# Optimization experiments

Measured on AMD Instinct MI355X. Metric: run time of the kernel, lower is better.

## Reference

```python
import jax, jax.numpy as jnp
import numpy as np
from jax import lax

B_COEF = np.array([0.0048243445989025905, 0.019297378395610362, 0.028946067593415543,
                   0.019297378395610362, 0.0048243445989025905], dtype=np.float32)
A_COEF = np.array([1.0, -2.369513007182038, 2.3139884144002064,
                   -1.0546654058785661, 0.18737949236818502], dtype=np.float32)


def setup_inputs() -> dict:
    key = jax.random.key(0)
    x = jax.random.normal(key, (32, 16, 32768), dtype=jnp.float32)
    return {"x": x, "b": jnp.asarray(B_COEF), "a": jnp.asarray(A_COEF)}


def _odd_ext(x, n):
    left = 2.0 * x[..., :1] - x[..., 1:n + 1][..., ::-1]
    right = 2.0 * x[..., -1:] - x[..., -(n + 1):-1][..., ::-1]
    return jnp.concatenate([left, x, right], axis=-1)


def _lfilter(x, b, a):
    # Direct form II transposed IIR, zero initial conditions.
    # x: [N, T]; b, a: [K]
    b = b / a[0]
    a = a / a[0]
    K = b.shape[0]

    def step(z, xt):  # z: [N, K-1], xt: [N]
        y = b[0] * xt + z[:, 0]
        z_shift = jnp.pad(z[:, 1:], ((0, 0), (0, 1)))
        z_new = b[1:] * xt[:, None] - a[1:] * y[:, None] + z_shift
        return z_new, y

    z0 = jnp.zeros((x.shape[0], K - 1), dtype=x.dtype)
    _, y = lax.scan(step, z0, x.T)  # y: [T, N]
    return y.T


def _filtfilt(x, b, a):
    # torchaudio-style filtfilt: forward lfilter, then backward lfilter (zero ICs).
    y = _lfilter(x, b, a)
    y = _lfilter(y[:, ::-1], b, a)[:, ::-1]
    return y


def reference(x, b, a):
    scale = jnp.max(jnp.abs(x), axis=-1, keepdims=True)
    xn = x / scale
    padlen = 3 * max(a.shape[0], b.shape[0])  # static: 15
    xe = _odd_ext(xn, padlen)                 # [B, C, T + 2*padlen]
    shp = xe.shape
    y = _filtfilt(xe.reshape(-1, shp[-1]), b, a)
    y = y.reshape(shp)[..., padlen:-padlen]
    return y * scale
```

## Files before the change

### kernel.cpp

```cpp
#include <hip/hip_runtime.h>


typedef __fp16 h2 __attribute__((ext_vector_type(2)));
typedef __fp16 h4 __attribute__((ext_vector_type(4)));
typedef __fp16 h8 __attribute__((ext_vector_type(8)));

constexpr int kT      = 32768;
constexpr int kSeg    = 2048;
constexpr int kNSeg   = kT / kSeg;
constexpr int kTPB    = 256;
constexpr int kSliceB = 4224;

#define B0 0.0048243445989025905f
#define B1 0.019297378395610362f
#define B2 0.028946067593415543f
#define B3 0.019297378395610362f
#define B4 0.0048243445989025905f
#define NA1 2.369513007182038f
#define NA2 (-2.3139884144002064f)
#define NA3 1.0546654058785661f
#define NA4 (-0.18737949236818502f)

#define STEPF(xv) do { \
    y  = fmaf(B0, (xv), z1); \
    z1 = fmaf(NA1, y, fmaf(B1, (xv), z2)); \
    z2 = fmaf(NA2, y, fmaf(B2, (xv), z3)); \
    z3 = fmaf(NA3, y, fmaf(B3, (xv), z4)); \
    z4 = fmaf(NA4, y, B4 * (xv)); \
} while (0)

#define PK(a, b) __builtin_bit_cast(int, __builtin_amdgcn_cvt_pkrtz((a), (b)))

__device__ __forceinline__ int swz(int lo) { return lo ^ (((lo >> 7) & 7) << 4); }

__global__ __launch_bounds__(kTPB, 4)
void filtfilt_kernel(const float* __restrict__ x, float* __restrict__ out) {
    __shared__ __align__(16) char lds[4 * kSliceB];
    const int t  = threadIdx.x;
    const int l  = t & 63;
    const int wv = t >> 6;
    const int W  = blockIdx.x * 4 + wv;
    const int row = W >> 4;
    const int seg = W & (kNSeg - 1);
    const float* __restrict__ xr   = x   + (size_t)row * kT + seg * kSeg;
    float* __restrict__ outr       = out + (size_t)row * kT + seg * kSeg;
    char* Lb = lds + wv * kSliceB;
    const bool haspre  = (seg > 0);
    const bool haspost = (seg < kNSeg - 1);

    const float4* xp = (const float4*)xr;
    float4 mv[8];
    #pragma unroll
    for (int i = 0; i < 8; ++i) mv[i] = xp[i * 64 + l];
    float4 pre4 = {0.f, 0.f, 0.f, 0.f}, post4 = {0.f, 0.f, 0.f, 0.f};
    if (l < 8) {
        if (haspre)  pre4  = *(const float4*)(xr - 32 + l * 4);
        if (haspost) post4 = *(const float4*)(xr + kSeg + l * 4);
    }
    #pragma unroll
    for (int i = 0; i < 8; ++i) {
        int lo = swz(64 + i * 512 + 8 * l);
        int2 wi = { PK(mv[i].x, mv[i].y), PK(mv[i].z, mv[i].w) };
        *(int2*)(Lb + lo) = wi;
    }
    if (l < 8) {
        if (haspre) {
            int2 wi = { PK(pre4.x, pre4.y), PK(pre4.z, pre4.w) };
            *(int2*)(Lb + 8 * l) = wi;
        }
        if (haspost) {
            int2 wi = { PK(post4.x, post4.y), PK(post4.z, post4.w) };
            *(int2*)(Lb + 4160 + 8 * l) = wi;
        }
    }
    asm volatile("s_waitcnt lgkmcnt(0)" ::: "memory");
    if (!haspre && l < 8) {
        const __fp16* xs = (const __fp16*)(Lb + 64);
        float x0 = (float)xs[0];
        float v[4];
        #pragma unroll
        for (int r = 0; r < 4; ++r) {
            int k = 4 * l + r;
            v[r] = (k < 17) ? 0.f : fmaf(2.f, x0, -(float)xs[32 - k]);
        }
        int2 wi = { PK(v[0], v[1]), PK(v[2], v[3]) };
        *(int2*)(Lb + 8 * l) = wi;
    }
    asm volatile("" ::: "memory");

    float z1 = 0.f, z2 = 0.f, z3 = 0.f, z4 = 0.f, y;
    {
        const int wb = l * 64;
        const int xv = ((wb >> 7) & 7) << 4;
        #pragma unroll
        for (int j = 0; j < 4; ++j) {
            h8 v = *(const h8*)(Lb + ((wb + 16 * j) ^ xv));
            #pragma unroll
            for (int e = 0; e < 8; ++e) STEPF((float)v[e]);
        }
    }

    h8 tailA, tailB;
    {
        const int mb = (l + 1) * 64;
        const int xm = ((mb >> 7) & 7) << 4;
        #pragma unroll
        for (int j = 0; j < 4; ++j) {
            char* p = Lb + ((mb + 16 * j) ^ xm);
            h8 v = *(const h8*)p;
            if (j == 2) tailA = v;
            if (j == 3) tailB = v;
            float q[8];
            #pragma unroll
            for (int e = 0; e < 8; ++e) { STEPF((float)v[e]); q[e] = y; }
            int4 wi = { PK(q[0], q[1]), PK(q[2], q[3]), PK(q[4], q[5]), PK(q[6], q[7]) };
            *(int4*)p = wi;
        }
    }

    if (l == 63) {
        if (haspost) {
            #pragma unroll
            for (int g = 0; g < 4; ++g) {
                h8 v = *(const h8*)(Lb + 4160 + 16 * g);
                if (g < 3) {
                    float q[8];
                    #pragma unroll
                    for (int e = 0; e < 8; ++e) { STEPF((float)v[e]); q[e] = y; }
                    int4 wi = { PK(q[0], q[1]), PK(q[2], q[3]), PK(q[4], q[5]), PK(q[6], q[7]) };
                    *(int4*)(Lb + 4160 + 16 * g) = wi;
                } else {
                    float q[4];
                    #pragma unroll
                    for (int e = 0; e < 4; ++e) { STEPF((float)v[e]); q[e] = y; }
                    int4 wi = { PK(q[0], q[1]), PK(q[2], q[3]), 0, 0 };
                    *(int4*)(Lb + 4160 + 16 * g) = wi;
                }
            }
        } else {
            float xl = (float)tailB[7];
            float q[8];
            #pragma unroll
            for (int j = 0; j < 8; ++j) {
                float xe = fmaf(2.f, xl, -(float)(j < 7 ? tailB[6 - j] : tailA[14 - j]));
                STEPF(xe); q[j] = y;
            }
            int4 w0 = { PK(q[0], q[1]), PK(q[2], q[3]), PK(q[4], q[5]), PK(q[6], q[7]) };
            *(int4*)(Lb + 4160) = w0;
            float r[7];
            #pragma unroll
            for (int j = 8; j < 15; ++j) {
                float xe = fmaf(2.f, xl, -(float)tailA[14 - j]);
                STEPF(xe); r[j - 8] = y;
            }
            int4 w1 = { PK(r[0], r[1]), PK(r[2], r[3]), PK(r[4], r[5]), PK(r[6], 0.f) };
            *(int4*)(Lb + 4176) = w1;
            int4 zz = {0, 0, 0, 0};
            *(int4*)(Lb + 4192) = zz;
            *(int4*)(Lb + 4208) = zz;
        }
    }
    asm volatile("" ::: "memory");

    z1 = z2 = z3 = z4 = 0.f;
    {
        const int bb = (l + 2) * 64;
        const int xb = ((bb >> 7) & 7) << 4;
        h8 w3v = *(const h8*)(Lb + ((bb + 48) ^ xb));
        h8 w2v = *(const h8*)(Lb + ((bb + 32) ^ xb));
        h8 w1v = *(const h8*)(Lb + ((bb + 16) ^ xb));
        h8 w0v = *(const h8*)(Lb + ((bb +  0) ^ xb));
        STEPF((float)w3v[3]); STEPF((float)w3v[2]);
        STEPF((float)w3v[1]); STEPF((float)w3v[0]);
        #pragma unroll
        for (int e = 7; e >= 0; --e) STEPF((float)w2v[e]);
        #pragma unroll
        for (int e = 7; e >= 0; --e) STEPF((float)w1v[e]);
        #pragma unroll
        for (int e = 7; e >= 0; --e) STEPF((float)w0v[e]);
    }

    {
        const int mb = (l + 1) * 64;
        const int xm = ((mb >> 7) & 7) << 4;
        #pragma unroll
        for (int j = 3; j >= 0; --j) {
            char* p = Lb + ((mb + 16 * j) ^ xm);
            h8 v = *(const h8*)p;
            float q[8];
            #pragma unroll
            for (int e = 7; e >= 0; --e) { STEPF((float)v[e]); q[e] = y; }
            int4 wi = { PK(q[0], q[1]), PK(q[2], q[3]), PK(q[4], q[5]), PK(q[6], q[7]) };
            *(int4*)p = wi;
        }
    }
    asm volatile("" ::: "memory");

    float4* op = (float4*)outr;
    #pragma unroll
    for (int i = 0; i < 8; ++i) {
        int lo = swz(64 + i * 512 + 8 * l);
        h4 hv = *(const h4*)(Lb + lo);
        float4 o = { (float)hv[0], (float)hv[1], (float)hv[2], (float)hv[3] };
        op[i * 64 + l] = o;
    }
}

extern "C" void kernel_launch(void* const* d_in, const int* in_sizes, int n_in,
                              void* d_out, int out_size, void* d_ws, size_t ws_size,
                              hipStream_t stream) {
    const float* x = (const float*)d_in[0];
    float* outp    = (float*)d_out;
    const int rows   = in_sizes[0] / kT;
    const int blocks = rows * kNSeg * 64 / kTPB;
    filtfilt_kernel<<<blocks, kTPB, 0, stream>>>(x, outp);
}
```

Measured before the change: 119.6 us.

## Process two segments per wave with second segment's loads issued upfront

Each wavefront now handles two adjacent 2048-sample segments instead of one, halving the grid size. Global loads for both segments are issued before the first segment's filtering so the second segment's memory latency hides behind the first's serial IIR compute. The cost is more live registers (a second set of eight float4 values) and fewer waves in flight, which may reduce occupancy-based latency hiding.

```diff
diff --git a/kernel.cpp b/kernel.cpp
--- a/kernel.cpp
+++ b/kernel.cpp
@@ -1,7 +1,6 @@
 #include <hip/hip_runtime.h>
 
 
-typedef __fp16 h2 __attribute__((ext_vector_type(2)));
 typedef __fp16 h4 __attribute__((ext_vector_type(4)));
 typedef __fp16 h8 __attribute__((ext_vector_type(8)));
 
@@ -33,30 +32,11 @@
 
 __device__ __forceinline__ int swz(int lo) { return lo ^ (((lo >> 7) & 7) << 4); }
 
-__global__ __launch_bounds__(kTPB, 4)
-void filtfilt_kernel(const float* __restrict__ x, float* __restrict__ out) {
-    __shared__ __align__(16) char lds[4 * kSliceB];
-    const int t  = threadIdx.x;
-    const int l  = t & 63;
-    const int wv = t >> 6;
-    const int W  = blockIdx.x * 4 + wv;
-    const int row = W >> 4;
-    const int seg = W & (kNSeg - 1);
-    const float* __restrict__ xr   = x   + (size_t)row * kT + seg * kSeg;
-    float* __restrict__ outr       = out + (size_t)row * kT + seg * kSeg;
-    char* Lb = lds + wv * kSliceB;
-    const bool haspre  = (seg > 0);
-    const bool haspost = (seg < kNSeg - 1);
-
-    const float4* xp = (const float4*)xr;
-    float4 mv[8];
-    #pragma unroll
-    for (int i = 0; i < 8; ++i) mv[i] = xp[i * 64 + l];
-    float4 pre4 = {0.f, 0.f, 0.f, 0.f}, post4 = {0.f, 0.f, 0.f, 0.f};
-    if (l < 8) {
-        if (haspre)  pre4  = *(const float4*)(xr - 32 + l * 4);
-        if (haspost) post4 = *(const float4*)(xr + kSeg + l * 4);
-    }
+__device__ __forceinline__ void process_seg(
+    char* __restrict__ Lb, const int l,
+    const float4 (&mv)[8], const float4 pre4, const float4 post4,
+    const bool haspre, const bool haspost, float* __restrict__ outr)
+{
     #pragma unroll
     for (int i = 0; i < 8; ++i) {
         int lo = swz(64 + i * 512 + 8 * l);
@@ -206,12 +186,53 @@
     }
 }
 
+__global__ __launch_bounds__(kTPB, 4)
+void filtfilt_kernel(const float* __restrict__ x, float* __restrict__ out) {
+    __shared__ __align__(16) char lds[4 * kSliceB];
+    const int t  = threadIdx.x;
+    const int l  = t & 63;
+    const int wv = t >> 6;
+    const int W  = blockIdx.x * 4 + wv;
+    const int row = W >> 3;
+    const int sp  = W & 7;
+    const int segA = 2 * sp;
+    const float* __restrict__ xrA = x + (size_t)row * kT + segA * kSeg;
+    const float* __restrict__ xrB = xrA + kSeg;
+    float* __restrict__ orA = out + (size_t)row * kT + segA * kSeg;
+    float* __restrict__ orB = orA + kSeg;
+    char* Lb = lds + wv * kSliceB;
+    const bool preA  = (segA > 0);
+    const bool postB = (sp < 7);
+
+    const float4* xpA = (const float4*)xrA;
+    const float4* xpB = (const float4*)xrB;
+    float4 mvA[8], mvB[8];
+    #pragma unroll
+    for (int i = 0; i < 8; ++i) mvA[i] = xpA[i * 64 + l];
+    float4 preA4 = {0.f,0.f,0.f,0.f}, postA4 = {0.f,0.f,0.f,0.f};
+    float4 preB4 = {0.f,0.f,0.f,0.f}, postB4 = {0.f,0.f,0.f,0.f};
+    if (l < 8) {
+        if (preA) preA4 = *(const float4*)(xrA - 32 + l * 4);
+        postA4 = *(const float4*)(xrA + kSeg + l * 4);
+        preB4  = *(const float4*)(xrB - 32 + l * 4);
+    }
+    #pragma unroll
+    for (int i = 0; i < 8; ++i) mvB[i] = xpB[i * 64 + l];
+    if (l < 8) {
+        if (postB) postB4 = *(const float4*)(xrB + kSeg + l * 4);
+    }
+    __builtin_amdgcn_sched_barrier(0);
+
+    process_seg(Lb, l, mvA, preA4, postA4, preA, true,  orA);
+    process_seg(Lb, l, mvB, preB4, postB4, true,  postB, orB);
+}
+
 extern "C" void kernel_launch(void* const* d_in, const int* in_sizes, int n_in,
                               void* d_out, int out_size, void* d_ws, size_t ws_size,
                               hipStream_t stream) {
     const float* x = (const float*)d_in[0];
     float* outp    = (float*)d_out;
     const int rows   = in_sizes[0] / kT;
-    const int blocks = rows * kNSeg * 64 / kTPB;
+    const int blocks = rows * (kNSeg / 2) * 64 / kTPB;
     filtfilt_kernel<<<blocks, kTPB, 0, stream>>>(x, outp);
 }
```

Measured after the change: 123.6 us. 3.4% more time.
